# Kernel tuning notes

Hardware: AMD Instinct MI355X
Metric: run time of the kernel (lower is better)

Reference implementation:

```python
import jax, jax.numpy as jnp
import numpy as np

TSTEPS = 20
THRES = 1.0
DECAY = (2**3 - 1) / 2**3  # 0.875, from mempot_decay=3

CH_IN, DIM_IN = 1, 64
C1, K1, D1 = 64, 7, 58    # 64 - 7 + 1
C2, K2, D2 = 128, 7, 52   # 58 - 7 + 1
NFLAT = C2 * D2 * D2      # 346112
NHID = 512
NOUT = 10


def _conv(x, w):
    # x: [1, Cin, H, W], w: [Cout, Cin, k, k] -> [1, Cout, H', W'] (VALID)
    return jax.lax.conv_general_dilated(
        x, w, window_strides=(1, 1), padding='VALID',
        dimension_numbers=('NCHW', 'OIHW', 'NCHW'))


def setup_inputs() -> dict:
    key = jax.random.key(0)
    k1, k2, k3, k4, k5 = jax.random.split(key, 5)
    image = jax.random.uniform(k1, (CH_IN, DIM_IN, DIM_IN), dtype=jnp.float32)
    # kaiming_normal_ fan_in init, matching nn.init.kaiming_normal_
    w_c1 = jax.random.normal(k2, (C1, CH_IN, K1, K1), jnp.float32) * np.sqrt(2.0 / (CH_IN * K1 * K1))
    w_c2 = jax.random.normal(k3, (C2, C1, K2, K2), jnp.float32) * np.sqrt(2.0 / (C1 * K2 * K2))
    w_l1 = jax.random.normal(k4, (NHID, NFLAT), jnp.float32) * np.sqrt(2.0 / NFLAT)
    w_l2 = jax.random.normal(k5, (NOUT, NHID), jnp.float32) * np.sqrt(2.0 / NHID)
    return {"image": image, "w_c1": w_c1, "w_c2": w_c2, "w_l1": w_l1, "w_l2": w_l2}


def reference(image, w_c1, w_c2, w_l1, w_l2):
    f32 = jnp.float32

    def step(carry, _):
        mp_in, mp_c1, sp_c1, mp_c2, sp_c2, mp_l1, sp_l1, mp_l2 = carry

        # --- SnnInput: integrate image, fire, subtract threshold (eval: no dropout)
        mp_in = mp_in + image
        fire_in = (mp_in >= THRES).astype(f32)
        mp_in = mp_in - THRES * fire_in
        s_in = fire_in  # spikes[tstep], read by conv1 this same tstep

        # --- SnnConv 1: reads input spikes at tstep
        mp_c1 = mp_c1 + _conv(s_in[None], w_c1)[0]
        f1 = (mp_c1 >= THRES).astype(f32)
        mp_c1 = (mp_c1 - THRES * f1) * jnp.where(f1 > 0, 1.0, DECAY)

        # --- SnnConv 2: reads conv1 spikes from PREVIOUS tstep (spikes[tstep])
        mp_c2 = mp_c2 + _conv(sp_c1[None], w_c2)[0]
        f2 = (mp_c2 >= THRES).astype(f32)
        mp_c2 = (mp_c2 - THRES * f2) * jnp.where(f2 > 0, 1.0, DECAY)

        # --- SnnFlatten: reads conv2 spikes from PREVIOUS tstep
        s_flat = sp_c2.reshape(-1)

        # --- SnnLinear 1 (hidden): decay first, then addmv (eval: no dropout)
        mp_l1 = mp_l1 * DECAY + w_l1 @ s_flat
        fl1 = (mp_l1 >= THRES).astype(f32)
        mp_l1 = mp_l1 - THRES * fl1

        # --- SnnLinear 2 (output): reads linear1 spikes from PREVIOUS tstep
        mp_l2 = mp_l2 * DECAY + w_l2 @ sp_l1
        fl2 = (mp_l2 >= THRES).astype(f32)
        mp_l2 = mp_l2 - THRES * fl2

        new_carry = (mp_in, mp_c1, f1, mp_c2, f2, mp_l1, fl1, mp_l2)
        return new_carry, fl2

    carry0 = (
        jnp.zeros((CH_IN, DIM_IN, DIM_IN), f32),
        jnp.zeros((C1, D1, D1), f32), jnp.zeros((C1, D1, D1), f32),
        jnp.zeros((C2, D2, D2), f32), jnp.zeros((C2, D2, D2), f32),
        jnp.zeros((NHID,), f32), jnp.zeros((NHID,), f32),
        jnp.zeros((NOUT,), f32),
    )
    _, spikes_out = jax.lax.scan(step, carry0, None, length=TSTEPS)
    # torch buffer has tsteps+1 rows; output layer writes index tstep+1, row 0 stays zero
    return jnp.concatenate([jnp.zeros((1, NOUT), f32), spikes_out], axis=0)
```

## Files before the change

kernel.cpp:

```cpp
#include <hip/hip_runtime.h>

#define TSTEPS 20
constexpr float THRES = 1.0f;
constexpr float DECAY = 0.875f;

constexpr int DIM_IN = 64;
constexpr int NIN = DIM_IN * DIM_IN;
constexpr int C1 = 64, K1 = 7, D1 = 58;
constexpr int N1 = C1 * D1 * D1;
constexpr int C2 = 128, K2 = 7, D2 = 52;
constexpr int N2 = C2 * D2 * D2;
constexpr int NFLAT = N2;
constexpr int NHID = 512;
constexpr int NOUT = 10;
constexpr int KC = 16;
constexpr int CPC = C1 / KC;
constexpr int W2R_ELEMS = 256 * 28 * 64;

constexpr int R_PART = 832;
constexpr int R_GATH = 768;
constexpr int R_RED = N2 / 256;
constexpr int R_C1 = C1;
constexpr int R_FIN = 8;
constexpr int B_GATH0 = R_PART;
constexpr int B_RED0 = B_GATH0 + R_GATH;
constexpr int B_C10 = B_RED0 + R_RED;
constexpr int B_FIN0 = B_C10 + R_C1;
constexpr int B_INPUT = B_FIN0 + R_FIN;
constexpr int B_LIN2 = B_INPUT + 1;
constexpr int B_MISC = B_LIN2 + 1;
constexpr int NBS = B_MISC + 1;

__device__ float g_mp_in[NIN];
__device__ float g_s_in[2][NIN];
__device__ float g_mp_c1[N1];
__device__ float g_sp_c1[2][N1];
__device__ float g_mp_c2[N2];
__device__ float g_sp_c2[N2];
__device__ float g_mp_l1[NHID];
__device__ float g_sp_l1[2][NHID];
__device__ float g_mp_l2[NOUT];
__device__ float g_dot[2][NHID];
__device__ double g_dotp[2][R_GATH][NHID];
__device__ int   g_nnz[4];
__device__ int   g_list[4][N2];
__device__ float g_part[2][KC * N2];
__device__ float g_w2r[W2R_ELEMS];

__global__ void init_kernel(const float* __restrict__ image, float* __restrict__ out) {
    int i = blockIdx.x * blockDim.x + threadIdx.x;
    int stride = gridDim.x * blockDim.x;
    for (int j = i; j < NIN; j += stride) {
        float mp = 2.f * image[j];
        float f = (mp >= THRES) ? 1.f : 0.f;
        g_mp_in[j] = mp - THRES * f;
        g_s_in[1][j] = f;
        g_s_in[0][j] = 0.f;
    }
    for (int j = i; j < N1; j += stride) {
        g_mp_c1[j] = 0.f; g_sp_c1[0][j] = 0.f; g_sp_c1[1][j] = 0.f;
    }
    for (int j = i; j < N2; j += stride) { g_mp_c2[j] = 0.f; g_sp_c2[j] = 0.f; }
    if (i < NHID) {
        g_mp_l1[i] = 0.f; g_sp_l1[0][i] = 0.f; g_sp_l1[1][i] = 0.f;
        g_dot[0][i] = 0.f; g_dot[1][i] = 0.f;
    }
    if (i < NOUT) g_mp_l2[i] = 0.f;
    if (i < (TSTEPS + 1) * NOUT) out[i] = 0.f;
    if (i < 4) g_nnz[i] = 0;
}

__global__ void __launch_bounds__(256) transpose_kernel(const float* __restrict__ w,
                                                        float* __restrict__ wT) {
    __shared__ float tile[64][65];
    int bx = blockIdx.x * 64;
    int by = blockIdx.y * 64;
    int tx = threadIdx.x & 63, ty = threadIdx.x >> 6;
#pragma unroll
    for (int k = 0; k < 16; ++k)
        tile[ty + 4 * k][tx] = w[(size_t)(by + ty + 4 * k) * NFLAT + bx + tx];
    __syncthreads();
#pragma unroll
    for (int k = 0; k < 16; ++k)
        wT[(size_t)(bx + ty + 4 * k) * NHID + by + tx] = tile[tx][ty + 4 * k];
}

__global__ void __launch_bounds__(256) reshuffle_w2(const float* __restrict__ w2) {
    int idx = blockIdx.x * 256 + threadIdx.x;
    if (idx >= C2 * C1 * 49) return;
    int co = idx / (C1 * 49);
    int rem = idx - co * (C1 * 49);
    int ci = rem / 49;
    int k = rem - ci * 49;
    int ky = k / 7, kx = k - ky * 7;
    int kc = ci >> 2, c = ci & 3;
    int cot = co >> 3, cl = co & 7;
    g_w2r[((size_t)(kc * 16 + cot) * 28 + (c * 7 + ky)) * 64 + cl * 8 + kx] = w2[idx];
}

__global__ void __launch_bounds__(256) step_kernel(const float* __restrict__ w1,
                                                   const float* __restrict__ wT,
                                                   const float* __restrict__ wl2,
                                                   const float* __restrict__ image,
                                                   float* __restrict__ out,
                                                   int k, int sparse) {
    __shared__ union __align__(16) {
        float spk[CPC][10][58];
        float sim[NIN];
        double fin[256];
        struct { int wcnt[4]; int base; } red;
    } sm;
    int bid = blockIdx.x, tid = threadIdx.x;
    int wid = tid >> 6, lane = tid & 63;

    if (bid < B_GATH0) {
        if (k < 2 || k > 17) return;
        int kc = bid & 15;
        int tmp = bid >> 4;
        int cotg = tmp & 3;
        int yt = tmp >> 2;
        int c0 = kc * CPC, y0 = yt * 4;
        const float* __restrict__ sp = g_sp_c1[(k + 1) & 1];
        for (int e = tid; e < CPC * 10 * 58; e += 256) {
            int c = e / 580, rem = e - c * 580;
            int r = rem / 58, x = rem - r * 58;
            sm.spk[c][r][x] = sp[(c0 + c) * (D1 * D1) + (y0 + r) * D1 + x];
        }
        __syncthreads();
        int cot = __builtin_amdgcn_readfirstlane(cotg * 4 + wid);
        int co0 = cot * 8;
        float acc[8][4] = {};
        bool act = lane < D2;
        float* __restrict__ pb = g_part[k & 1];
#pragma unroll 1
        for (int c = 0; c < CPC; ++c) {
#pragma unroll
            for (int ky = 0; ky < K2; ++ky) {
                float v[4][7];
                if (act) {
#pragma unroll
                    for (int o = 0; o < 4; ++o)
#pragma unroll
                        for (int kx = 0; kx < 7; ++kx)
                            v[o][kx] = sm.spk[c][o + ky][lane + kx];
                }
                const float* __restrict__ wrow =
                    g_w2r + ((size_t)(kc * 16 + cot) * 28 + (c * 7 + ky)) * 64;
#pragma unroll
                for (int cl = 0; cl < 8; ++cl) {
                    float wv[7];
#pragma unroll
                    for (int kx = 0; kx < 7; ++kx) wv[kx] = wrow[cl * 8 + kx];
                    if (act) {
#pragma unroll
                        for (int o = 0; o < 4; ++o)
#pragma unroll
                            for (int kx = 0; kx < 7; ++kx)
                                acc[cl][o] = fmaf(v[o][kx], wv[kx], acc[cl][o]);
                    }
                }
            }
        }
        if (act) {
#pragma unroll
            for (int cl = 0; cl < 8; ++cl)
#pragma unroll
                for (int o = 0; o < 4; ++o)
                    pb[(size_t)kc * N2 + (co0 + cl) * (D2 * D2) + (y0 + o) * D2 + lane] =
                        acc[cl][o];
        }
    } else if (bid < B_RED0) {
        if (!sparse || k < 4 || k > 19) return;
        int s = k - 1;
        int gb = bid - B_GATH0;
        int ps = (s - 1) & 3;
        int nnz = g_nnz[ps];
        const int* __restrict__ list = g_list[ps];
        const float2* __restrict__ wT2 = (const float2*)wT;
        int h = tid;
        double ax[8] = {}, ay[8] = {};
        int i = gb;
        for (; i + 7 * R_GATH < nnz; i += 8 * R_GATH) {
            int j[8];
#pragma unroll
            for (int u = 0; u < 8; ++u) j[u] = list[i + u * R_GATH];
#pragma unroll
            for (int u = 0; u < 8; ++u) {
                float2 w = wT2[(size_t)j[u] * 256 + h];
                ax[u] += w.x; ay[u] += w.y;
            }
        }
        for (; i < nnz; i += R_GATH) {
            float2 w = wT2[(size_t)list[i] * 256 + h];
            ax[0] += w.x; ay[0] += w.y;
        }
        g_dotp[s & 1][gb][2 * h] =
            ((ax[0] + ax[1]) + (ax[2] + ax[3])) + ((ax[4] + ax[5]) + (ax[6] + ax[7]));
        g_dotp[s & 1][gb][2 * h + 1] =
            ((ay[0] + ay[1]) + (ay[2] + ay[3])) + ((ay[4] + ay[5]) + (ay[6] + ay[7]));
    } else if (bid < B_C10) {
        if (k < 3 || k > 18) return;
        int s = k - 1;
        int i = (bid - B_RED0) * 256 + tid;
        const float* __restrict__ pb = g_part[s & 1];
        float sum = 0.f;
#pragma unroll
        for (int kk = 0; kk < KC; ++kk) sum += pb[(size_t)kk * N2 + i];
        float mp = g_mp_c2[i] + sum;
        float f = (mp >= THRES) ? 1.f : 0.f;
        g_mp_c2[i] = (mp - THRES * f) * ((f > 0.f) ? 1.f : DECAY);
        if (!sparse) g_sp_c2[i] = f;
        bool spike = f > 0.f;
        unsigned long long m = __ballot(spike);
        int lpre = __popcll(m & ((1ull << lane) - 1));
        if (lane == 0) sm.red.wcnt[wid] = __popcll(m);
        __syncthreads();
        int w0 = sm.red.wcnt[0], w1c = sm.red.wcnt[1],
            w2c = sm.red.wcnt[2], w3c = sm.red.wcnt[3];
        int total = w0 + w1c + w2c + w3c;
        if (tid == 0 && total > 0)
            sm.red.base = atomicAdd(&g_nnz[s & 3], total);
        __syncthreads();
        if (spike) {
            int woff = (wid > 0 ? w0 : 0) + (wid > 1 ? w1c : 0) + (wid > 2 ? w2c : 0);
            g_list[s & 3][sm.red.base + woff + lpre] = i;
        }
    } else if (bid < B_FIN0) {
        if (k < 1 || k > 16) return;
        int co = bid - B_C10;
        const float4* __restrict__ s4 = (const float4*)g_s_in[k & 1];
        float4* d4 = (float4*)sm.sim;
        for (int j = tid; j < NIN / 4; j += 256) d4[j] = s4[j];
        __syncthreads();
        float w[49];
#pragma unroll
        for (int kk = 0; kk < 49; ++kk) w[kk] = w1[co * 49 + kk];
        float* __restrict__ spb = g_sp_c1[k & 1];
        for (int idx = tid; idx < D1 * D1; idx += 256) {
            int y = idx / D1, x = idx - y * D1;
            float a = 0.f;
#pragma unroll
            for (int ky = 0; ky < K1; ++ky)
#pragma unroll
                for (int kx = 0; kx < K1; ++kx)
                    a = fmaf(sm.sim[(y + ky) * DIM_IN + x + kx], w[ky * K1 + kx], a);
            int o = co * (D1 * D1) + idx;
            float mp = g_mp_c1[o] + a;
            float f = (mp >= THRES) ? 1.f : 0.f;
            g_mp_c1[o] = (mp - THRES * f) * ((f > 0.f) ? 1.f : DECAY);
            spb[o] = f;
        }
    } else if (bid < B_INPUT) {
        if (k < 5 || k > 20) return;
        int s = k - 2;
        int fb = bid - B_FIN0;
        int hl = tid & 63, wch = tid >> 6;
        int h = fb * 64 + hl;
        float tot;
        if (sparse) {
            int p = s & 1;
            double sum = 0.0;
            int b0 = wch * (R_GATH / 4);
            for (int b = b0; b < b0 + R_GATH / 4; ++b) sum += g_dotp[p][b][h];
            sm.fin[wch * 64 + hl] = sum;
            __syncthreads();
            if (wch != 0) return;
            tot = (float)((sm.fin[hl] + sm.fin[64 + hl]) +
                          (sm.fin[128 + hl] + sm.fin[192 + hl]));
        } else {
            if (wch != 0) return;
            tot = g_dot[s & 1][h];
        }
        float mp = g_mp_l1[h] * DECAY + tot;
        float f = (mp >= THRES) ? 1.f : 0.f;
        g_mp_l1[h] = mp - THRES * f;
        g_sp_l1[s & 1][h] = f;
    } else if (bid == B_INPUT) {
        if (k < 1 || k > 15) return;
        int s = k + 1;
        float* __restrict__ sb = g_s_in[s & 1];
        for (int j = tid; j < NIN; j += 256) {
            float mp = g_mp_in[j] + image[j];
            float f = (mp >= THRES) ? 1.f : 0.f;
            sb[j] = f;
            g_mp_in[j] = mp - THRES * f;
        }
    } else if (bid == B_LIN2) {
        if (k < 6 || k > 21) return;
        int s = k - 2;
        const float* __restrict__ sl = g_sp_l1[(s - 1) & 1];
        for (int o = wid; o < NOUT; o += 4) {
            float a = 0.f;
#pragma unroll
            for (int kk = lane; kk < NHID; kk += 64)
                a = fmaf(wl2[o * NHID + kk], sl[kk], a);
            for (int off = 32; off; off >>= 1) a += __shfl_down(a, off, 64);
            if (lane == 0) {
                float mp = g_mp_l2[o] * DECAY + a;
                float f = (mp >= THRES) ? 1.f : 0.f;
                g_mp_l2[o] = mp - THRES * f;
                out[(s + 1) * NOUT + o] = f;
            }
        }
    } else {
        if (k < 2 || k > 17) return;
        if (tid == 0) g_nnz[k & 3] = 0;
    }
}

__global__ void __launch_bounds__(256) linear1_dense(const float* __restrict__ wl1,
                                                     int slot) {
    int row = blockIdx.x;
    const float4* __restrict__ w4 = (const float4*)(wl1 + (size_t)row * NFLAT);
    const float4* __restrict__ s4 = (const float4*)g_sp_c2;
    float acc = 0.f;
    for (int j = threadIdx.x; j < NFLAT / 4; j += 256) {
        float4 w = w4[j];
        float4 s = s4[j];
        acc += w.x * s.x + w.y * s.y + w.z * s.z + w.w * s.w;
    }
    __shared__ float red[256];
    red[threadIdx.x] = acc;
    __syncthreads();
    for (int off = 128; off >= 1; off >>= 1) {
        if (threadIdx.x < off) red[threadIdx.x] += red[threadIdx.x + off];
        __syncthreads();
    }
    if (threadIdx.x == 0) g_dot[slot][row] = red[0];
}

extern "C" void kernel_launch(void* const* d_in, const int* in_sizes, int n_in,
                              void* d_out, int out_size, void* d_ws, size_t ws_size,
                              hipStream_t stream) {
    const float* image = (const float*)d_in[0];
    const float* w_c1 = (const float*)d_in[1];
    const float* w_c2 = (const float*)d_in[2];
    const float* w_l1 = (const float*)d_in[3];
    const float* w_l2 = (const float*)d_in[4];
    float* out = (float*)d_out;

    float* wT = (float*)d_ws;
    bool sparse = ws_size >= (size_t)NFLAT * NHID * sizeof(float);

    init_kernel<<<512, 256, 0, stream>>>(image, out);
    reshuffle_w2<<<(C2 * C1 * 49) / 256, 256, 0, stream>>>(w_c2);
    if (sparse)
        transpose_kernel<<<dim3(NFLAT / 64, NHID / 64), 256, 0, stream>>>(w_l1, wT);

    for (int k = 1; k <= 21; ++k) {
        step_kernel<<<NBS, 256, 0, stream>>>(w_c1, wT, w_l2, image, out, k,
                                             sparse ? 1 : 0);
        if (!sparse && k >= 3 && k <= 18)
            linear1_dense<<<NHID, 256, 0, stream>>>(w_l1, k & 1);
    }
}
```

Measured before the change: 1.710 ms.

## Fold weight transpose and reshuffle into early step launches, retile conv2 waves

The separate transpose kernel for the linear1 weights and the conv2 weight reshuffle kernel are removed. That work now runs as extra blocks inside the first three step launches, so it overlaps with the light early-timestep work instead of running serially before it. Block indices are permuted with a prime stride so the different roles interleave across CUs. The conv2 tile is also reshaped: each wave now covers 16 output channels by 2 rows instead of 8 channels by 4 rows, which changes the balance between weight loads and spike-tile loads and the register use. The risk is that the extra blocks and the permutation raise contention during the early steps.

```diff
diff --git a/kernel.cpp b/kernel.cpp
--- a/kernel.cpp
+++ b/kernel.cpp
@@ -15,21 +15,23 @@
 constexpr int NOUT = 10;
 constexpr int KC = 16;
 constexpr int CPC = C1 / KC;
-constexpr int W2R_ELEMS = 256 * 28 * 64;
-
-constexpr int R_PART = 832;
+constexpr int W2R_ELEMS = 16 * 8 * 28 * 128;
+
 constexpr int R_GATH = 768;
 constexpr int R_RED = N2 / 256;
-constexpr int R_C1 = C1;
-constexpr int R_FIN = 8;
-constexpr int B_GATH0 = R_PART;
+constexpr int B_GATH0 = 832;
 constexpr int B_RED0 = B_GATH0 + R_GATH;
 constexpr int B_C10 = B_RED0 + R_RED;
-constexpr int B_FIN0 = B_C10 + R_C1;
-constexpr int B_INPUT = B_FIN0 + R_FIN;
+constexpr int B_FIN0 = B_C10 + C1;
+constexpr int B_INPUT = B_FIN0 + 8;
 constexpr int B_LIN2 = B_INPUT + 1;
 constexpr int B_MISC = B_LIN2 + 1;
 constexpr int NBS = B_MISC + 1;
+constexpr int NT = 1803;
+constexpr int B_TR0 = NBS;
+constexpr int B_RSH0 = NBS + NT;
+constexpr int NBS_T = B_RSH0 + 64;
+constexpr int PERM = 1031;
 
 __device__ float g_mp_in[NIN];
 __device__ float g_s_in[2][NIN];
@@ -70,35 +72,9 @@
     if (i < 4) g_nnz[i] = 0;
 }
 
-__global__ void __launch_bounds__(256) transpose_kernel(const float* __restrict__ w,
-                                                        float* __restrict__ wT) {
-    __shared__ float tile[64][65];
-    int bx = blockIdx.x * 64;
-    int by = blockIdx.y * 64;
-    int tx = threadIdx.x & 63, ty = threadIdx.x >> 6;
-#pragma unroll
-    for (int k = 0; k < 16; ++k)
-        tile[ty + 4 * k][tx] = w[(size_t)(by + ty + 4 * k) * NFLAT + bx + tx];
-    __syncthreads();
-#pragma unroll
-    for (int k = 0; k < 16; ++k)
-        wT[(size_t)(bx + ty + 4 * k) * NHID + by + tx] = tile[tx][ty + 4 * k];
-}
-
-__global__ void __launch_bounds__(256) reshuffle_w2(const float* __restrict__ w2) {
-    int idx = blockIdx.x * 256 + threadIdx.x;
-    if (idx >= C2 * C1 * 49) return;
-    int co = idx / (C1 * 49);
-    int rem = idx - co * (C1 * 49);
-    int ci = rem / 49;
-    int k = rem - ci * 49;
-    int ky = k / 7, kx = k - ky * 7;
-    int kc = ci >> 2, c = ci & 3;
-    int cot = co >> 3, cl = co & 7;
-    g_w2r[((size_t)(kc * 16 + cot) * 28 + (c * 7 + ky)) * 64 + cl * 8 + kx] = w2[idx];
-}
-
 __global__ void __launch_bounds__(256) step_kernel(const float* __restrict__ w1,
+                                                   const float* __restrict__ w2full,
+                                                   const float* __restrict__ wl1,
                                                    const float* __restrict__ wT,
                                                    const float* __restrict__ wl2,
                                                    const float* __restrict__ image,
@@ -109,16 +85,19 @@
         float sim[NIN];
         double fin[256];
         struct { int wcnt[4]; int base; } red;
+        float tile[64][65];
     } sm;
-    int bid = blockIdx.x, tid = threadIdx.x;
+    int grid = (k <= 3) ? NBS_T : NBS;
+    int nb = (int)(((long long)blockIdx.x * PERM) % grid);
+    int tid = threadIdx.x;
     int wid = tid >> 6, lane = tid & 63;
 
-    if (bid < B_GATH0) {
+    if (nb < B_GATH0) {
         if (k < 2 || k > 17) return;
-        int kc = bid & 15;
-        int tmp = bid >> 4;
-        int cotg = tmp & 3;
-        int yt = tmp >> 2;
+        int kc = nb & 15;
+        int q = nb >> 4;
+        int coq = q & 3;
+        int yt = q >> 2;
         int c0 = kc * CPC, y0 = yt * 4;
         const float* __restrict__ sp = g_sp_c1[(k + 1) & 1];
         for (int e = tid; e < CPC * 10 * 58; e += 256) {
@@ -127,52 +106,53 @@
             sm.spk[c][r][x] = sp[(c0 + c) * (D1 * D1) + (y0 + r) * D1 + x];
         }
         __syncthreads();
-        int cot = __builtin_amdgcn_readfirstlane(cotg * 4 + wid);
-        int co0 = cot * 8;
-        float acc[8][4] = {};
+        int coh = wid & 1, oh = wid >> 1;
+        int cot16 = __builtin_amdgcn_readfirstlane(coq * 2 + coh);
+        int co0 = cot16 * 16;
+        float acc[16][2] = {};
         bool act = lane < D2;
         float* __restrict__ pb = g_part[k & 1];
 #pragma unroll 1
         for (int c = 0; c < CPC; ++c) {
 #pragma unroll
             for (int ky = 0; ky < K2; ++ky) {
-                float v[4][7];
+                float v[2][7];
                 if (act) {
 #pragma unroll
-                    for (int o = 0; o < 4; ++o)
+                    for (int dy = 0; dy < 2; ++dy)
 #pragma unroll
                         for (int kx = 0; kx < 7; ++kx)
-                            v[o][kx] = sm.spk[c][o + ky][lane + kx];
+                            v[dy][kx] = sm.spk[c][2 * oh + dy + ky][lane + kx];
                 }
                 const float* __restrict__ wrow =
-                    g_w2r + ((size_t)(kc * 16 + cot) * 28 + (c * 7 + ky)) * 64;
-#pragma unroll
-                for (int cl = 0; cl < 8; ++cl) {
+                    g_w2r + ((size_t)(kc * 8 + cot16) * 28 + (c * 7 + ky)) * 128;
+#pragma unroll
+                for (int cl = 0; cl < 16; ++cl) {
                     float wv[7];
 #pragma unroll
                     for (int kx = 0; kx < 7; ++kx) wv[kx] = wrow[cl * 8 + kx];
                     if (act) {
 #pragma unroll
-                        for (int o = 0; o < 4; ++o)
+                        for (int dy = 0; dy < 2; ++dy)
 #pragma unroll
                             for (int kx = 0; kx < 7; ++kx)
-                                acc[cl][o] = fmaf(v[o][kx], wv[kx], acc[cl][o]);
+                                acc[cl][dy] = fmaf(v[dy][kx], wv[kx], acc[cl][dy]);
                     }
                 }
             }
         }
         if (act) {
 #pragma unroll
-            for (int cl = 0; cl < 8; ++cl)
-#pragma unroll
-                for (int o = 0; o < 4; ++o)
-                    pb[(size_t)kc * N2 + (co0 + cl) * (D2 * D2) + (y0 + o) * D2 + lane] =
-                        acc[cl][o];
-        }
-    } else if (bid < B_RED0) {
+            for (int cl = 0; cl < 16; ++cl)
+#pragma unroll
+                for (int dy = 0; dy < 2; ++dy)
+                    pb[(size_t)kc * N2 + (co0 + cl) * (D2 * D2) +
+                       (y0 + 2 * oh + dy) * D2 + lane] = acc[cl][dy];
+        }
+    } else if (nb < B_RED0) {
         if (!sparse || k < 4 || k > 19) return;
         int s = k - 1;
-        int gb = bid - B_GATH0;
+        int gb = nb - B_GATH0;
         int ps = (s - 1) & 3;
         int nnz = g_nnz[ps];
         const int* __restrict__ list = g_list[ps];
@@ -198,10 +178,10 @@
             ((ax[0] + ax[1]) + (ax[2] + ax[3])) + ((ax[4] + ax[5]) + (ax[6] + ax[7]));
         g_dotp[s & 1][gb][2 * h + 1] =
             ((ay[0] + ay[1]) + (ay[2] + ay[3])) + ((ay[4] + ay[5]) + (ay[6] + ay[7]));
-    } else if (bid < B_C10) {
+    } else if (nb < B_C10) {
         if (k < 3 || k > 18) return;
         int s = k - 1;
-        int i = (bid - B_RED0) * 256 + tid;
+        int i = (nb - B_RED0) * 256 + tid;
         const float* __restrict__ pb = g_part[s & 1];
         float sum = 0.f;
 #pragma unroll
@@ -225,9 +205,9 @@
             int woff = (wid > 0 ? w0 : 0) + (wid > 1 ? w1c : 0) + (wid > 2 ? w2c : 0);
             g_list[s & 3][sm.red.base + woff + lpre] = i;
         }
-    } else if (bid < B_FIN0) {
+    } else if (nb < B_FIN0) {
         if (k < 1 || k > 16) return;
-        int co = bid - B_C10;
+        int co = nb - B_C10;
         const float4* __restrict__ s4 = (const float4*)g_s_in[k & 1];
         float4* d4 = (float4*)sm.sim;
         for (int j = tid; j < NIN / 4; j += 256) d4[j] = s4[j];
@@ -250,10 +230,10 @@
             g_mp_c1[o] = (mp - THRES * f) * ((f > 0.f) ? 1.f : DECAY);
             spb[o] = f;
         }
-    } else if (bid < B_INPUT) {
+    } else if (nb < B_INPUT) {
         if (k < 5 || k > 20) return;
         int s = k - 2;
-        int fb = bid - B_FIN0;
+        int fb = nb - B_FIN0;
         int hl = tid & 63, wch = tid >> 6;
         int h = fb * 64 + hl;
         float tot;
@@ -275,7 +255,7 @@
         float f = (mp >= THRES) ? 1.f : 0.f;
         g_mp_l1[h] = mp - THRES * f;
         g_sp_l1[s & 1][h] = f;
-    } else if (bid == B_INPUT) {
+    } else if (nb == B_INPUT) {
         if (k < 1 || k > 15) return;
         int s = k + 1;
         float* __restrict__ sb = g_s_in[s & 1];
@@ -285,7 +265,7 @@
             sb[j] = f;
             g_mp_in[j] = mp - THRES * f;
         }
-    } else if (bid == B_LIN2) {
+    } else if (nb == B_LIN2) {
         if (k < 6 || k > 21) return;
         int s = k - 2;
         const float* __restrict__ sl = g_sp_l1[(s - 1) & 1];
@@ -302,9 +282,44 @@
                 out[(s + 1) * NOUT + o] = f;
             }
         }
-    } else {
+    } else if (nb == B_MISC) {
         if (k < 2 || k > 17) return;
         if (tid == 0) g_nnz[k & 3] = 0;
+    } else if (nb < B_RSH0) {
+        if (!sparse || k > 3) return;
+        int sg = (nb - B_TR0) + (k - 1) * NT;
+        if (sg >= NFLAT / 64) return;
+        int bx = sg * 64;
+        int tx = tid & 63, ty = tid >> 6;
+        float* __restrict__ wTm = (float*)wT;
+#pragma unroll 1
+        for (int rt = 0; rt < NHID / 64; ++rt) {
+            int by = rt * 64;
+#pragma unroll
+            for (int kk = 0; kk < 16; ++kk)
+                sm.tile[ty + 4 * kk][tx] =
+                    wl1[(size_t)(by + ty + 4 * kk) * NFLAT + bx + tx];
+            __syncthreads();
+#pragma unroll
+            for (int kk = 0; kk < 16; ++kk)
+                wTm[(size_t)(bx + ty + 4 * kk) * NHID + by + tx] =
+                    sm.tile[tx][ty + 4 * kk];
+            __syncthreads();
+        }
+    } else {
+        if (k != 1) return;
+        int rb = nb - B_RSH0;
+        for (int idx = rb * 256 + tid; idx < C2 * C1 * 49; idx += 64 * 256) {
+            int co = idx / (C1 * 49);
+            int rem = idx - co * (C1 * 49);
+            int ci = rem / 49;
+            int kk2 = rem - ci * 49;
+            int ky = kk2 / 7, kx = kk2 - ky * 7;
+            int kc = ci >> 2, c = ci & 3;
+            int cot16 = co >> 4, cl = co & 15;
+            g_w2r[((size_t)(kc * 8 + cot16) * 28 + (c * 7 + ky)) * 128 + cl * 8 + kx] =
+                w2full[idx];
+        }
     }
 }
 
@@ -343,13 +358,11 @@
     bool sparse = ws_size >= (size_t)NFLAT * NHID * sizeof(float);
 
     init_kernel<<<512, 256, 0, stream>>>(image, out);
-    reshuffle_w2<<<(C2 * C1 * 49) / 256, 256, 0, stream>>>(w_c2);
-    if (sparse)
-        transpose_kernel<<<dim3(NFLAT / 64, NHID / 64), 256, 0, stream>>>(w_l1, wT);
 
     for (int k = 1; k <= 21; ++k) {
-        step_kernel<<<NBS, 256, 0, stream>>>(w_c1, wT, w_l2, image, out, k,
-                                             sparse ? 1 : 0);
+        int grid = (k <= 3) ? NBS_T : NBS;
+        step_kernel<<<grid, 256, 0, stream>>>(w_c1, w_c2, w_l1, wT, w_l2, image,
+                                              out, k, sparse ? 1 : 0);
         if (!sparse && k >= 3 && k <= 18)
             linear1_dense<<<NHID, 256, 0, stream>>>(w_l1, k & 1);
     }
```

After: 3.103 ms. 81.4% more time.
